# Kernel optimization log

Measured on AMD Instinct MI355X. Metric: run time of the kernel, lower is better.

The kernel has to match this reference:

```python
import jax, jax.numpy as jnp
import numpy as np

# dims
N_USER = 30000; N_ITEM = 30000; HID = 256; HEADS = 4; DH = HID // HEADS
L = 2; E_BUYS = 200000
IMG_D = 512; TASTE_D = 768; NUTR_D = 20; LR = 64; IMG_RANK = 64
EPS = 1e-5
# node type order: 0=user 1=item 2=taste 3=intention 4=image
# edge type order: taste->item, intention->item, image->item, user->item (buys), item->user (bought_by)


def _bn(x, g, b):
    # nn.BatchNorm1d in training mode (biased variance), deterministic
    mu = jnp.mean(x, axis=0)
    var = jnp.mean((x - mu) ** 2, axis=0)
    return (x - mu) * jax.lax.rsqrt(var + EPS) * g + b


def _segment_softmax(logits, seg, n):
    m = jax.ops.segment_max(logits, seg, num_segments=n)
    m = jnp.where(jnp.isfinite(m), m, 0.0)
    e = jnp.exp(logits - m[seg])
    s = jax.ops.segment_sum(e, seg, num_segments=n)
    return e / (s[seg] + 1e-16)


def _model(p, user_id, item_id, buys_src, buys_dst):
    # --- encoders (dropout = identity in eval) ---
    xu = jax.nn.relu(_bn(p['user_emb'][user_id] @ p['user_W'] + p['user_b'], p['user_bn_g'], p['user_bn_b']))
    xi = jax.nn.relu(_bn(p['item_emb'][item_id] @ p['item_W'] + p['item_b'], p['item_bn_g'], p['item_bn_b']))
    ximg = (p['image_feat'] @ p['img_U']) @ p['img_V'] + p['img_b']  # LowRankLinear
    xt = p['taste_feat'] @ p['taste_W'] + p['taste_b']
    xn = p['intent_feat'] @ p['intent_W'] + p['intent_b']
    xs = [xu, xi, xt, xn, ximg]
    assoc = jnp.arange(N_ITEM, dtype=jnp.int32)
    # (src_type, dst_type, src_idx, dst_idx)
    edges = [(2, 1, assoc, assoc), (3, 1, assoc, assoc), (4, 1, assoc, assoc),
             (0, 1, buys_src, buys_dst), (1, 0, buys_dst, buys_src)]
    scale = 1.0 / np.sqrt(DH)
    n_of = [N_USER, N_ITEM]
    for l in range(L):
        k, q, v = [], [], []
        for t in range(5):
            kqv = xs[t] @ p['kqv_W'][l, t] + p['kqv_b'][l, t]
            kk, qq, vv = jnp.split(kqv, 3, axis=1)
            k.append(kk.reshape(-1, HEADS, DH))
            q.append(qq.reshape(-1, HEADS, DH))
            v.append(vv.reshape(-1, HEADS, DH))
        buf = {0: [], 1: []}
        for e, (s, d, si, di) in enumerate(edges):
            # relation-specific per-head transforms of source k/v (all src nodes, then gather)
            ke = jnp.einsum('nhd,hde->nhe', k[s], p['k_rel'][l, e])
            ve = jnp.einsum('nhd,hde->nhe', v[s], p['v_rel'][l, e])
            logit = jnp.sum(q[d][di] * ke[si], axis=-1) * p['p_rel'][l, e] * scale  # [E,H]
            buf[d].append((logit, ve[si], di))
        new_xs = list(xs)
        for d in (0, 1):  # dst node types: user, item
            logits = jnp.concatenate([b[0] for b in buf[d]], axis=0)
            msgs = jnp.concatenate([b[1] for b in buf[d]], axis=0)
            dsts = jnp.concatenate([b[2] for b in buf[d]], axis=0)
            alpha = _segment_softmax(logits, dsts, n_of[d])  # softmax over ALL incoming edges per dst node
            agg = jax.ops.segment_sum(alpha[:, :, None] * msgs, dsts, num_segments=n_of[d])
            o = jax.nn.gelu(agg.reshape(-1, HID), approximate=False) @ p['out_W'][l, d] + p['out_b'][l, d]
            sg = jax.nn.sigmoid(p['skip'][l, d])
            o = sg * o + (1.0 - sg) * xs[d]  # HGTConv learned skip
            o = o + xs[d]                    # MultiModalFusionGAT residual
            o = jax.nn.relu(_bn(o, p['fbn_g'][l, d], p['fbn_b'][l, d]))  # per-type BN+ReLU (dropout eval)
            new_xs[d] = o
        xs = new_xs  # taste/intention/image pass through unchanged
    return jnp.stack(xs, axis=0)  # [5, 30000, HID]


def setup_inputs():
    key = jax.random.key(0)
    ks = iter(jax.random.split(key, 48))
    def nrm(shape, scale=0.05):
        return jax.random.normal(next(ks), shape, dtype=jnp.float32) * scale
    z = lambda *s: jnp.zeros(s, jnp.float32)
    o = lambda *s: jnp.ones(s, jnp.float32)
    inp = {}
    inp['user_id'] = jnp.arange(N_USER, dtype=jnp.int32)
    inp['item_id'] = jnp.arange(N_ITEM, dtype=jnp.int32)
    inp['buys_src'] = jax.random.randint(next(ks), (E_BUYS,), 0, N_USER, dtype=jnp.int32)
    inp['buys_dst'] = jax.random.randint(next(ks), (E_BUYS,), 0, N_ITEM, dtype=jnp.int32)
    inp['image_feat'] = nrm((N_ITEM, IMG_D), 1.0)
    inp['taste_feat'] = nrm((N_ITEM, TASTE_D), 1.0)
    inp['intent_feat'] = nrm((N_ITEM, NUTR_D), 1.0)
    inp['user_emb'] = nrm((N_USER, LR), 0.1)
    inp['user_W'] = nrm((LR, HID)); inp['user_b'] = z(HID)
    inp['user_bn_g'] = o(HID); inp['user_bn_b'] = z(HID)
    inp['item_emb'] = nrm((N_ITEM, LR), 0.1)
    inp['item_W'] = nrm((LR, HID)); inp['item_b'] = z(HID)
    inp['item_bn_g'] = o(HID); inp['item_bn_b'] = z(HID)
    inp['img_U'] = nrm((IMG_D, IMG_RANK)); inp['img_V'] = nrm((IMG_RANK, HID)); inp['img_b'] = z(HID)
    inp['taste_W'] = nrm((TASTE_D, HID)); inp['taste_b'] = z(HID)
    inp['intent_W'] = nrm((NUTR_D, HID)); inp['intent_b'] = z(HID)
    inp['kqv_W'] = nrm((L, 5, HID, 3 * HID)); inp['kqv_b'] = z(L, 5, 3 * HID)
    inp['out_W'] = nrm((L, 5, HID, HID)); inp['out_b'] = z(L, 5, HID)
    inp['k_rel'] = nrm((L, 5, HEADS, DH, DH))
    inp['v_rel'] = nrm((L, 5, HEADS, DH, DH))
    inp['p_rel'] = o(L, 5, HEADS)
    inp['skip'] = o(L, 5)
    inp['fbn_g'] = o(L, 2, HID); inp['fbn_b'] = z(L, 2, HID)
    return inp


def reference(user_id, item_id, buys_src, buys_dst, image_feat, taste_feat, intent_feat,
              user_emb, user_W, user_b, user_bn_g, user_bn_b,
              item_emb, item_W, item_b, item_bn_g, item_bn_b,
              img_U, img_V, img_b, taste_W, taste_b, intent_W, intent_b,
              kqv_W, kqv_b, out_W, out_b, k_rel, v_rel, p_rel, skip, fbn_g, fbn_b):
    p = dict(image_feat=image_feat, taste_feat=taste_feat, intent_feat=intent_feat,
             user_emb=user_emb, user_W=user_W, user_b=user_b, user_bn_g=user_bn_g, user_bn_b=user_bn_b,
             item_emb=item_emb, item_W=item_W, item_b=item_b, item_bn_g=item_bn_g, item_bn_b=item_bn_b,
             img_U=img_U, img_V=img_V, img_b=img_b, taste_W=taste_W, taste_b=taste_b,
             intent_W=intent_W, intent_b=intent_b, kqv_W=kqv_W, kqv_b=kqv_b, out_W=out_W, out_b=out_b,
             k_rel=k_rel, v_rel=v_rel, p_rel=p_rel, skip=skip, fbn_g=fbn_g, fbn_b=fbn_b)
    return _model(p, user_id, item_id, buys_src, buys_dst)
```

## Files before the change

### kernel.cpp

```cpp
#include <hip/hip_runtime.h>
#include <math.h>

#define HID 256
#define EBUY 200000
#define NNODE 30000
#define MP 30080
static const size_t S  = (size_t)NNODE * HID;
static const size_t SP = (size_t)MP * HID;

typedef __attribute__((ext_vector_type(8))) short  short8;
typedef __attribute__((ext_vector_type(4))) float  f32x4;

#define OFF_TASTE 0
#define OFF_INT   196608
#define OFF_IMGU  204800
#define OFF_IMGV  237568
#define OFF_USER  253952
#define OFF_ITEM  270336
#define OFF_OUTW  286720
#define WENC_TOT  548864

__device__ __forceinline__ float gelu_f(float x) {
    return 0.5f * x * (1.0f + erff(x * 0.70710678118654752f));
}
__device__ __forceinline__ unsigned short f2bf(float f) {
    unsigned u = __float_as_uint(f);
    u = (u + 0x7FFFu + ((u >> 16) & 1u)) >> 16;
    return (unsigned short)u;
}
__device__ __forceinline__ float b2f(unsigned short us) {
    return __uint_as_float((unsigned)us << 16);
}

__global__ void conv_pad(const float* __restrict__ in, unsigned short* __restrict__ o,
                         int M, int K, int Kpad)
{
    int i = blockIdx.x * 256 + threadIdx.x;
    if (i >= M * Kpad) return;
    int r = i / Kpad, k = i % Kpad;
    o[i] = (k < K) ? f2bf(in[(size_t)r * K + k]) : (unsigned short)0;
}

__global__ void wtconv_all(const float* __restrict__ taste_W, const float* __restrict__ intent_W,
                           const float* __restrict__ img_U, const float* __restrict__ img_V,
                           const float* __restrict__ user_W, const float* __restrict__ item_W,
                           const float* __restrict__ out_W, unsigned short* __restrict__ WENC)
{
    int i = blockIdx.x * 256 + threadIdx.x;
    if (i >= WENC_TOT) return;
    const float* W; int K, N, Kpad, idx;
    if (i < OFF_INT)        { W = taste_W;  K = 768; N = 256; Kpad = 768; idx = i - OFF_TASTE; }
    else if (i < OFF_IMGU)  { W = intent_W; K = 20;  N = 256; Kpad = 32;  idx = i - OFF_INT; }
    else if (i < OFF_IMGV)  { W = img_U;    K = 512; N = 64;  Kpad = 512; idx = i - OFF_IMGU; }
    else if (i < OFF_USER)  { W = img_V;    K = 64;  N = 256; Kpad = 64;  idx = i - OFF_IMGV; }
    else if (i < OFF_ITEM)  { W = user_W;   K = 64;  N = 256; Kpad = 64;  idx = i - OFF_USER; }
    else if (i < OFF_OUTW)  { W = item_W;   K = 64;  N = 256; Kpad = 64;  idx = i - OFF_ITEM; }
    else {
        int k = (i - OFF_OUTW) >> 16;
        int l = k >> 1, d = k & 1;
        W = out_W + (size_t)(l * 5 + d) * 65536;
        K = 256; N = 256; Kpad = 256; idx = (i - OFF_OUTW) & 65535;
    }
    int n = idx / Kpad, kk = idx % Kpad;
    WENC[i] = (kk < K) ? f2bf(W[(size_t)kk * N + n]) : (unsigned short)0;
}

__global__ void build_kqv(const float* __restrict__ kqv_W, const float* __restrict__ kqv_b,
                          const float* __restrict__ k_rel, const float* __restrict__ v_rel,
                          unsigned short* __restrict__ WKV, float* __restrict__ bKV,
                          unsigned short* __restrict__ WQ, float* __restrict__ bQ)
{
    int s = blockIdx.y;
    int l = s / 5, t = s % 5;
    static const int es[5] = {3, 4, 0, 1, 2};
    int e = es[t];
    int tid = blockIdx.x * 256 + threadIdx.x;
    if (tid >= 257 * 768) return;
    int r = tid / 768, c = tid % 768;
    int cb = c >> 8, cc = c & 255;
    int h = cc >> 6, dd = cc & 63;
    const float* W = kqv_W + (size_t)s * 196608;
    const float* bv = kqv_b + (size_t)s * 768;
    const float* Wrow = (r < 256) ? (W + (size_t)r * 768) : bv;
    if (cb == 1) {
        if (t >= 2) return;
        float outv = Wrow[256 + cc];
        if (r < 256) WQ[(size_t)(l * 2 + t) * 65536 + (size_t)cc * 256 + r] = f2bf(outv);
        else         bQ[(l * 2 + t) * 256 + cc] = outv;
        return;
    }
    const float* R = ((cb == 0) ? k_rel : v_rel) + (size_t)(l * 5 + e) * 16384 + (size_t)h * 4096;
    int sb = (cb == 0) ? 0 : 512;
    float sum = 0.f;
    #pragma unroll 8
    for (int d = 0; d < 64; ++d)
        sum += Wrow[sb + h * 64 + d] * R[d * 64 + dd];
    int col = (cb == 0) ? cc : 256 + cc;
    if (r < 256) WKV[(size_t)s * 131072 + (size_t)col * 256 + r] = f2bf(sum);
    else         bKV[s * 512 + col] = sum;
}

#define KPAD 40
#define OPAD 136
template<int AF32, int GATH2, int BSEL, int EPI>
__launch_bounds__(256)
__global__ void gemm_mfma(const void* __restrict__ Ap, const void* __restrict__ Ap2,
                          const int* __restrict__ g1, const int* __restrict__ g2,
                          const unsigned short* __restrict__ BT0, int bStride,
                          const float* __restrict__ bias0, const float* __restrict__ bias1,
                          int biasStride,
                          float* __restrict__ D0, unsigned short* __restrict__ Db,
                          unsigned short* __restrict__ Db2,
                          int M, int N, int K,
                          const float* __restrict__ skipP, const float* __restrict__ resid,
                          float* __restrict__ bns)
{
    __shared__ union {
        struct { unsigned short A[128 * KPAD]; unsigned short B[128 * KPAD]; } s;
        unsigned short O[128 * OPAD];
    } sm;
    const int tid = threadIdx.x;
    const int gx = gridDim.x;
    int bid = blockIdx.y * gx + blockIdx.x;
    {
        int nwg = gx * gridDim.y;
        int q = nwg >> 3, r = nwg & 7;
        int xc = bid & 7, i = bid >> 3;
        int base = (xc < r) ? xc * (q + 1) : r * (q + 1) + (xc - r) * q;
        bid = base + i;
    }
    const int bx = bid % gx, by = bid / gx;
    const int row0 = by * 128, col0 = bx * 128;
    const int wid = tid >> 6, lane = tid & 63;
    const int wr = wid >> 1, wc = wid & 1;
    const int l16 = lane & 15, kg = lane >> 4;
    const int tt = (BSEL || GATH2) ? (by / 235) : 0;

    const unsigned short* BT = BT0 + (size_t)tt * bStride;
    const float* bias = bias0;
    if (GATH2)              bias = tt ? bias1 : bias0;
    else if (BSEL && bias0) bias = bias0 + (size_t)tt * biasStride;

    f32x4 acc[4][4];
    const f32x4 zero = {0.f, 0.f, 0.f, 0.f};
    #pragma unroll
    for (int i = 0; i < 4; ++i)
        #pragma unroll
        for (int j = 0; j < 4; ++j) acc[i][j] = zero;

    const int rA0 = tid >> 2, rA1 = (tid + 256) >> 2;
    const int q0 = tid & 3;

    const float* Af0 = nullptr; const float* Af1 = nullptr;
    const unsigned short* Ab0 = nullptr; const unsigned short* Ab1 = nullptr;
    if (GATH2) {
        int lr0 = row0 + rA0 - tt * MP; if (lr0 >= NNODE) lr0 = NNODE - 1;
        int lr1 = row0 + rA1 - tt * MP; if (lr1 >= NNODE) lr1 = NNODE - 1;
        const int* gA = tt ? g2 : g1;
        const float* Abase = tt ? (const float*)Ap2 : (const float*)Ap;
        Af0 = Abase + (size_t)gA[lr0] * K;
        Af1 = Abase + (size_t)gA[lr1] * K;
    } else if (AF32) {
        Af0 = (const float*)Ap + (size_t)min(row0 + rA0, M - 1) * K;
        Af1 = (const float*)Ap + (size_t)min(row0 + rA1, M - 1) * K;
    } else {
        Ab0 = (const unsigned short*)Ap + (size_t)min(row0 + rA0, M - 1) * K;
        Ab1 = (const unsigned short*)Ap + (size_t)min(row0 + rA1, M - 1) * K;
    }
    const unsigned short* Bb0 = BT + (size_t)min(col0 + rA0, N - 1) * K;
    const unsigned short* Bb1 = BT + (size_t)min(col0 + rA1, N - 1) * K;

    for (int k0 = 0; k0 < K; k0 += 32) {
        if (AF32 || GATH2) {
            float4 x0 = *(const float4*)&Af0[k0 + q0 * 8];
            float4 x1 = *(const float4*)&Af0[k0 + q0 * 8 + 4];
            float4 y0 = *(const float4*)&Af1[k0 + q0 * 8];
            float4 y1 = *(const float4*)&Af1[k0 + q0 * 8 + 4];
            ushort4 u0 = {f2bf(x0.x), f2bf(x0.y), f2bf(x0.z), f2bf(x0.w)};
            ushort4 u1 = {f2bf(x1.x), f2bf(x1.y), f2bf(x1.z), f2bf(x1.w)};
            ushort4 w0 = {f2bf(y0.x), f2bf(y0.y), f2bf(y0.z), f2bf(y0.w)};
            ushort4 w1 = {f2bf(y1.x), f2bf(y1.y), f2bf(y1.z), f2bf(y1.w)};
            *(ushort4*)&sm.s.A[rA0 * KPAD + q0 * 8]     = u0;
            *(ushort4*)&sm.s.A[rA0 * KPAD + q0 * 8 + 4] = u1;
            *(ushort4*)&sm.s.A[rA1 * KPAD + q0 * 8]     = w0;
            *(ushort4*)&sm.s.A[rA1 * KPAD + q0 * 8 + 4] = w1;
        } else {
            *(uint4*)&sm.s.A[rA0 * KPAD + q0 * 8] = *(const uint4*)&Ab0[k0 + q0 * 8];
            *(uint4*)&sm.s.A[rA1 * KPAD + q0 * 8] = *(const uint4*)&Ab1[k0 + q0 * 8];
        }
        *(uint4*)&sm.s.B[rA0 * KPAD + q0 * 8] = *(const uint4*)&Bb0[k0 + q0 * 8];
        *(uint4*)&sm.s.B[rA1 * KPAD + q0 * 8] = *(const uint4*)&Bb1[k0 + q0 * 8];
        __syncthreads();
        short8 af[4], bfr[4];
        #pragma unroll
        for (int i = 0; i < 4; ++i) {
            af[i]  = *(const short8*)&sm.s.A[(wr * 64 + i * 16 + l16) * KPAD + kg * 8];
            bfr[i] = *(const short8*)&sm.s.B[(wc * 64 + i * 16 + l16) * KPAD + kg * 8];
        }
        #pragma unroll
        for (int i = 0; i < 4; ++i)
            #pragma unroll
            for (int j = 0; j < 4; ++j)
                acc[i][j] = __builtin_amdgcn_mfma_f32_16x16x32_bf16(af[i], bfr[j], acc[i][j], 0, 0, 0);
        __syncthreads();
    }

    float sg = 0.f;
    if (EPI == 2) sg = 1.f / (1.f + __expf(-skipP[0]));
    #pragma unroll
    for (int j = 0; j < 4; ++j) {
        int lc = wc * 64 + j * 16 + l16;
        int cc = col0 + lc;
        float cs = 0.f, cs2 = 0.f;
        float bv = (bias && cc < N) ? bias[cc] : 0.f;
        #pragma unroll
        for (int i = 0; i < 4; ++i) {
            #pragma unroll
            for (int r = 0; r < 4; ++r) {
                int lr = wr * 64 + i * 16 + kg * 4 + r;
                int rr = row0 + lr;
                float v = acc[i][j][r] + bv;
                if (EPI == 0) {
                    if (D0 && cc < N && rr < M) D0[(size_t)rr * N + cc] = v;
                    sm.O[lr * OPAD + lc] = f2bf(v);
                } else if (EPI == 4 || EPI == 5) {
                    sm.O[lr * OPAD + lc] = f2bf(v);
                } else if (EPI == 6) {
                    D0[(size_t)rr * 256 + cc] = v;
                } else if (EPI == 2) {
                    if (rr < M) {
                        float xo = resid[(size_t)rr * 256 + cc];
                        float o = sg * v + (2.f - sg) * xo;
                        D0[(size_t)rr * 256 + cc] = o;
                        cs += o; cs2 += o * o;
                    }
                }
            }
        }
        if (EPI == 2) {
            cs  += __shfl_xor(cs, 16);  cs  += __shfl_xor(cs, 32);
            cs2 += __shfl_xor(cs2, 16); cs2 += __shfl_xor(cs2, 32);
            if (kg == 0 && cc < N) {
                atomicAdd(&bns[cc], cs);
                atomicAdd(&bns[256 + cc], cs2);
            }
        }
    }
    if (EPI == 0 || EPI == 4 || EPI == 5) {
        __syncthreads();
        unsigned short* T; int ldN, cofs;
        if (EPI == 4)      { T = (col0 < 256) ? Db : Db2; ldN = 256; cofs = col0 & 255; }
        else if (EPI == 5) { T = Db; ldN = 256; cofs = col0; }
        else               { T = Db; ldN = N;   cofs = col0; }
        int nloc = N - col0; if (nloc > 128) nloc = 128;
        if (nloc >= 128) {
            int lr = tid >> 1, half = tid & 1;
            int rr = row0 + lr;
            if (EPI != 0 || rr < M) {
                uint4* dst = (uint4*)&T[(size_t)rr * ldN + cofs + half * 64];
                const uint4* srcp = (const uint4*)&sm.O[lr * OPAD + half * 64];
                #pragma unroll
                for (int c = 0; c < 8; ++c) dst[c] = srcp[c];
            }
        } else {
            if (tid < 128) {
                int lr = tid, rr = row0 + lr;
                if (rr < M) {
                    uint4* dst = (uint4*)&T[(size_t)rr * ldN + cofs];
                    const uint4* srcp = (const uint4*)&sm.O[lr * OPAD];
                    #pragma unroll
                    for (int c = 0; c < 8; ++c) dst[c] = srcp[c];
                }
            }
        }
    }
}

__global__ void edge_hist2(const int* __restrict__ dstk, const int* __restrict__ srck,
                           int* __restrict__ cnt)
{
    int j = blockIdx.x * 256 + threadIdx.x;
    if (j < EBUY) atomicAdd(&cnt[dstk[j]], 1);
    else if (j < 2 * EBUY) atomicAdd(&cnt[NNODE + srck[j - EBUY]], 1);
}

#define SCAN_NB 30
#define SCAN_CH 1000
__global__ void scan_part(const int* __restrict__ cnt, int* __restrict__ bt)
{
    int set = blockIdx.y;
    const int* c = cnt + set * NNODE;
    int b = blockIdx.x;
    int i = b * SCAN_CH + threadIdx.x;
    int v = (threadIdx.x < SCAN_CH && i < NNODE) ? c[i] : 0;
    __shared__ int wsum[16];
    int lane = threadIdx.x & 63, wv = threadIdx.x >> 6;
    for (int o = 32; o; o >>= 1) v += __shfl_down(v, o);
    if (lane == 0) wsum[wv] = v;
    __syncthreads();
    if (threadIdx.x == 0) {
        int s = 0;
        for (int w = 0; w < 16; ++w) s += wsum[w];
        bt[set * 32 + b] = s;
    }
}

__global__ void scan_mid(int* __restrict__ bt, int* __restrict__ off_i, int* __restrict__ off_u)
{
    int set = threadIdx.x;
    if (set >= 2) return;
    int* b = bt + set * 32;
    int s = 0;
    for (int i = 0; i < SCAN_NB; ++i) { int c = b[i]; b[i] = s; s += c; }
    (set ? off_u : off_i)[NNODE] = s;
}

__global__ void scan_final(const int* __restrict__ cnt, const int* __restrict__ bt,
                           int* __restrict__ off_i, int* __restrict__ off_u,
                           int* __restrict__ cur_i, int* __restrict__ cur_u)
{
    int set = blockIdx.y;
    const int* c = cnt + set * NNODE;
    int* off = set ? off_u : off_i;
    int* cur = set ? cur_u : cur_i;
    int b = blockIdx.x;
    int i = b * SCAN_CH + threadIdx.x;
    int v = (threadIdx.x < SCAN_CH && i < NNODE) ? c[i] : 0;
    int lane = threadIdx.x & 63, wv = threadIdx.x >> 6;
    int x = v;
    for (int o = 1; o < 64; o <<= 1) { int t = __shfl_up(x, o); if (lane >= o) x += t; }
    __shared__ int wtot[16];
    if (lane == 63) wtot[wv] = x;
    __syncthreads();
    if (wv == 0) {
        int y = (lane < 16) ? wtot[lane] : 0;
        for (int o = 1; o < 16; o <<= 1) { int t = __shfl_up(y, o); if (lane >= o) y += t; }
        if (lane < 16) wtot[lane] = y;
    }
    __syncthreads();
    int wbase = (wv == 0) ? 0 : wtot[wv - 1];
    int excl = bt[set * 32 + b] + wbase + x - v;
    if (threadIdx.x < SCAN_CH && i < NNODE) { off[i] = excl; cur[i] = excl; }
}

__global__ void edge_place2(const int* __restrict__ dstk, const int* __restrict__ srck,
                            int* __restrict__ cur_i, int* __restrict__ cur_u,
                            int* __restrict__ src_i, int* __restrict__ src_u)
{
    int j = blockIdx.x * 256 + threadIdx.x;
    if (j < EBUY) {
        int pos = atomicAdd(&cur_i[dstk[j]], 1);
        src_i[pos] = srck[j];
    } else if (j < 2 * EBUY) {
        int j2 = j - EBUY;
        int pos = atomicAdd(&cur_u[srck[j2]], 1);
        src_u[pos] = dstk[j2];
    }
}

template<int HAS_ASSOC>
__launch_bounds__(256)
__global__ void attn_gather(const unsigned short* __restrict__ Qd,
                            const unsigned short* __restrict__ KEs,
                            const unsigned short* __restrict__ VEs,
                            const unsigned short* __restrict__ KEa,
                            const unsigned short* __restrict__ VEa,
                            const int* __restrict__ roff, const int* __restrict__ srcArr,
                            const float* __restrict__ pR,
                            unsigned short* __restrict__ AGGb)
{
    int wid = (blockIdx.x * 256 + threadIdx.x) >> 6;
    int lane = threadIdx.x & 63;
    if (wid >= NNODE) return;
    int h = lane >> 4;

    ushort4 qb = *(const ushort4*)(Qd + (size_t)wid * 256 + lane * 4);
    float4 q = {b2f(qb.x), b2f(qb.y), b2f(qb.z), b2f(qb.w)};
    float m = -INFINITY, s = 0.f;
    float4 acc = {0.f, 0.f, 0.f, 0.f};

    if (HAS_ASSOC) {
        #pragma unroll
        for (int e = 0; e < 3; ++e) {
            ushort4 kb = *(const ushort4*)(KEa + (size_t)e * SP + (size_t)wid * 256 + lane * 4);
            float d = q.x * b2f(kb.x) + q.y * b2f(kb.y) + q.z * b2f(kb.z) + q.w * b2f(kb.w);
            for (int off = 8; off; off >>= 1) d += __shfl_xor(d, off, 16);
            float lg = d * pR[e * 4 + h] * 0.125f;
            ushort4 vv = *(const ushort4*)(VEa + (size_t)e * SP + (size_t)wid * 256 + lane * 4);
            float mn = fmaxf(m, lg);
            float so = __expf(m - mn);
            float ev = __expf(lg - mn);
            s = s * so + ev;
            acc.x = acc.x * so + ev * b2f(vv.x);
            acc.y = acc.y * so + ev * b2f(vv.y);
            acc.z = acc.z * so + ev * b2f(vv.z);
            acc.w = acc.w * so + ev * b2f(vv.w);
            m = mn;
        }
    }

    float pb = pR[(HAS_ASSOC ? 12 : 16) + h] * 0.125f;
    int j1 = roff[wid + 1];
    for (int j = roff[wid]; j < j1; ++j) {
        int src = srcArr[j];
        ushort4 kb = *(const ushort4*)(KEs + (size_t)src * 256 + lane * 4);
        float d = q.x * b2f(kb.x) + q.y * b2f(kb.y) + q.z * b2f(kb.z) + q.w * b2f(kb.w);
        for (int off = 8; off; off >>= 1) d += __shfl_xor(d, off, 16);
        float lg = d * pb;
        ushort4 vv = *(const ushort4*)(VEs + (size_t)src * 256 + lane * 4);
        float mn = fmaxf(m, lg);
        float so = __expf(m - mn);
        float ev = __expf(lg - mn);
        s = s * so + ev;
        acc.x = acc.x * so + ev * b2f(vv.x);
        acc.y = acc.y * so + ev * b2f(vv.y);
        acc.z = acc.z * so + ev * b2f(vv.z);
        acc.w = acc.w * so + ev * b2f(vv.w);
        m = mn;
    }

    float inv = 1.f / (s + 1e-16f);
    ushort4 o4;
    o4.x = f2bf(gelu_f(acc.x * inv));
    o4.y = f2bf(gelu_f(acc.y * inv));
    o4.z = f2bf(gelu_f(acc.z * inv));
    o4.w = f2bf(gelu_f(acc.w * inv));
    *(ushort4*)(AGGb + (size_t)wid * 256 + lane * 4) = o4;
}

#define BNB 512
__global__ void bn_stats2(const float* __restrict__ SCRf, float* __restrict__ part)
{
    int tt = blockIdx.y;
    const float* x = SCRf + (size_t)tt * SP;
    int col = threadIdx.x;
    int b = blockIdx.x;
    float s = 0.f, s2 = 0.f;
    int r = b;
    for (; r + 3 * BNB < NNODE; r += 4 * BNB) {
        float v0 = x[(size_t)r * 256 + col];
        float v1 = x[(size_t)(r + BNB) * 256 + col];
        float v2 = x[(size_t)(r + 2 * BNB) * 256 + col];
        float v3 = x[(size_t)(r + 3 * BNB) * 256 + col];
        s += v0 + v1 + v2 + v3;
        s2 += v0 * v0 + v1 * v1 + v2 * v2 + v3 * v3;
    }
    for (; r < NNODE; r += BNB) {
        float v = x[(size_t)r * 256 + col];
        s += v; s2 += v * v;
    }
    part[((size_t)tt * BNB + b) * 512 + col] = s;
    part[((size_t)tt * BNB + b) * 512 + 256 + col] = s2;
}

__global__ void bn_fin2(const float* __restrict__ part,
                        const float* __restrict__ g0, const float* __restrict__ b0,
                        const float* __restrict__ g1, const float* __restrict__ b1,
                        float* __restrict__ scsh)
{
    int tid = threadIdx.x;
    int tt = tid >> 8, col = tid & 255;
    const float* p = part + (size_t)tt * BNB * 512;
    float s = 0.f, s2 = 0.f;
    #pragma unroll 4
    for (int b = 0; b < BNB; ++b) { s += p[b * 512 + col]; s2 += p[b * 512 + 256 + col]; }
    float mu = s / (float)NNODE;
    float var = s2 / (float)NNODE - mu * mu;
    float sc = rsqrtf(var + 1e-5f) * (tt ? g1 : g0)[col];
    scsh[tt * 512 + col] = sc;
    scsh[tt * 512 + 256 + col] = (tt ? b1 : b0)[col] - mu * sc;
}

__global__ void bn_apply2(const float* __restrict__ SCRf, const float* __restrict__ scsh,
                          float* __restrict__ out, unsigned short* __restrict__ XBall)
{
    const int Q4 = NNODE * 64;
    for (int i = blockIdx.x * 256 + threadIdx.x; i < 2 * Q4; i += gridDim.x * 256) {
        int tt = (i >= Q4) ? 1 : 0;
        int local = i - tt * Q4;
        int c4 = local & 63;
        float4 sc4 = *(const float4*)&scsh[tt * 512 + c4 * 4];
        float4 sh4 = *(const float4*)&scsh[tt * 512 + 256 + c4 * 4];
        float4 v = ((const float4*)(SCRf + (size_t)tt * SP))[local];
        v.x = fmaxf(v.x * sc4.x + sh4.x, 0.f);
        v.y = fmaxf(v.y * sc4.y + sh4.y, 0.f);
        v.z = fmaxf(v.z * sc4.z + sh4.z, 0.f);
        v.w = fmaxf(v.w * sc4.w + sh4.w, 0.f);
        ((float4*)(out + (size_t)tt * S))[local] = v;
        ushort4 u = {f2bf(v.x), f2bf(v.y), f2bf(v.z), f2bf(v.w)};
        ((ushort4*)(XBall + (size_t)tt * SP))[local] = u;
    }
}

__global__ void bn_find(const float* __restrict__ bns, const float* __restrict__ g,
                        const float* __restrict__ b_, float* __restrict__ scsh)
{
    int col = threadIdx.x;
    float s = bns[col], s2 = bns[256 + col];
    float mu = s / (float)NNODE;
    float var = s2 / (float)NNODE - mu * mu;
    float sc = rsqrtf(var + 1e-5f) * g[col];
    scsh[col] = sc;
    scsh[256 + col] = b_[col] - mu * sc;
}

__global__ void bn_apply1(const float* __restrict__ x, const float* __restrict__ scsh,
                          float* __restrict__ y, unsigned short* __restrict__ yb)
{
    const int Q4 = NNODE * 64;
    int c4 = threadIdx.x & 63;
    float4 sc4 = *(const float4*)&scsh[c4 * 4];
    float4 sh4 = *(const float4*)&scsh[256 + c4 * 4];
    for (int i = blockIdx.x * 256 + threadIdx.x; i < Q4; i += gridDim.x * 256) {
        float4 v = ((const float4*)x)[i];
        v.x = fmaxf(v.x * sc4.x + sh4.x, 0.f);
        v.y = fmaxf(v.y * sc4.y + sh4.y, 0.f);
        v.z = fmaxf(v.z * sc4.z + sh4.z, 0.f);
        v.w = fmaxf(v.w * sc4.w + sh4.w, 0.f);
        ((float4*)y)[i] = v;
        ushort4 u = {f2bf(v.x), f2bf(v.y), f2bf(v.z), f2bf(v.w)};
        ((ushort4*)yb)[i] = u;
    }
}

extern "C" void kernel_launch(void* const* d_in, const int* in_sizes, int n_in,
                              void* d_out, int out_size, void* d_ws, size_t ws_size,
                              hipStream_t stream)
{
    const int*   user_id    = (const int*)d_in[0];
    const int*   item_id    = (const int*)d_in[1];
    const int*   buys_src   = (const int*)d_in[2];
    const int*   buys_dst   = (const int*)d_in[3];
    const float* image_feat = (const float*)d_in[4];
    const float* taste_feat = (const float*)d_in[5];
    const float* intent_feat= (const float*)d_in[6];
    const float* user_emb   = (const float*)d_in[7];
    const float* user_W     = (const float*)d_in[8];
    const float* user_b     = (const float*)d_in[9];
    const float* user_bn_g  = (const float*)d_in[10];
    const float* user_bn_b  = (const float*)d_in[11];
    const float* item_emb   = (const float*)d_in[12];
    const float* item_W     = (const float*)d_in[13];
    const float* item_b     = (const float*)d_in[14];
    const float* item_bn_g  = (const float*)d_in[15];
    const float* item_bn_b  = (const float*)d_in[16];
    const float* img_U      = (const float*)d_in[17];
    const float* img_V      = (const float*)d_in[18];
    const float* img_b      = (const float*)d_in[19];
    const float* taste_W    = (const float*)d_in[20];
    const float* taste_b    = (const float*)d_in[21];
    const float* intent_W   = (const float*)d_in[22];
    const float* intent_b   = (const float*)d_in[23];
    const float* kqv_W      = (const float*)d_in[24];
    const float* kqv_b      = (const float*)d_in[25];
    const float* out_W      = (const float*)d_in[26];
    const float* out_b      = (const float*)d_in[27];
    const float* k_rel      = (const float*)d_in[28];
    const float* v_rel      = (const float*)d_in[29];
    const float* p_rel      = (const float*)d_in[30];
    const float* skip       = (const float*)d_in[31];
    const float* fbn_g      = (const float*)d_in[32];
    const float* fbn_b      = (const float*)d_in[33];

    float* out = (float*)d_out;
    float* ws  = (float*)d_ws;

    float* SCRf = ws;
    float* BNSp = SCRf + 2 * SP;
    float* BNS  = BNSp + 2 * BNB * 512;
    float* SCSH = BNS + 512;
    float* bKV  = SCSH + 1024;
    float* bQ   = bKV + 5120;
    unsigned short* QB    = (unsigned short*)(bQ + 1024);
    unsigned short* XBall = QB + 2 * SP;
    unsigned short* KEall = XBall + 5 * SP;
    unsigned short* VEall = KEall + 5 * SP;
    unsigned short* AGB   = VEall + 5 * SP;
    unsigned short* IMB   = AGB + S;
    unsigned short* IPB   = IMB + (size_t)NNODE * 64;
    unsigned short* WKV   = IPB + (size_t)NNODE * 32;
    unsigned short* WQ    = WKV + 1310720;
    unsigned short* WENC  = WQ + 262144;
    int* cnt   = (int*)(WENC + WENC_TOT);
    int* off_i = cnt + 2 * NNODE;
    int* off_u = off_i + NNODE + 1;
    int* cur_i = off_u + NNODE + 1;
    int* cur_u = cur_i + NNODE;
    int* src_i = cur_u + NNODE;
    int* src_u = src_i + EBUY;
    int* bt    = src_u + EBUY;

    size_t need = (size_t)((char*)(bt + 64) - (char*)ws);
    if (ws_size < need) return;

    hipMemsetAsync(cnt, 0, 2 * NNODE * 4, stream);
    edge_hist2<<<(2 * EBUY + 255) / 256, 256, 0, stream>>>(buys_dst, buys_src, cnt);
    scan_part<<<dim3(SCAN_NB, 2), 1024, 0, stream>>>(cnt, bt);
    scan_mid<<<1, 64, 0, stream>>>(bt, off_i, off_u);
    scan_final<<<dim3(SCAN_NB, 2), 1024, 0, stream>>>(cnt, bt, off_i, off_u, cur_i, cur_u);
    edge_place2<<<(2 * EBUY + 255) / 256, 256, 0, stream>>>(buys_dst, buys_src, cur_i, cur_u, src_i, src_u);

    wtconv_all<<<(WENC_TOT + 255) / 256, 256, 0, stream>>>(taste_W, intent_W, img_U, img_V,
                                                           user_W, item_W, out_W, WENC);
    build_kqv<<<dim3(771, 10), 256, 0, stream>>>(kqv_W, kqv_b, k_rel, v_rel, WKV, bKV, WQ, bQ);
    conv_pad<<<(NNODE * 32 + 255) / 256, 256, 0, stream>>>(intent_feat, IPB, NNODE, 20, 32);

    hipLaunchKernelGGL((gemm_mfma<1,0,0,0>), dim3(2,235), dim3(256), 0, stream,
        taste_feat, nullptr, nullptr, nullptr, WENC + OFF_TASTE, 0, taste_b, nullptr, 0,
        out + 2*S, XBall + 2*SP, nullptr, NNODE, 256, 768, nullptr, nullptr, nullptr);
    hipLaunchKernelGGL((gemm_mfma<0,0,0,0>), dim3(2,235), dim3(256), 0, stream,
        IPB, nullptr, nullptr, nullptr, WENC + OFF_INT, 0, intent_b, nullptr, 0,
        out + 3*S, XBall + 3*SP, nullptr, NNODE, 256, 32, nullptr, nullptr, nullptr);
    hipLaunchKernelGGL((gemm_mfma<1,0,0,0>), dim3(1,235), dim3(256), 0, stream,
        image_feat, nullptr, nullptr, nullptr, WENC + OFF_IMGU, 0, nullptr, nullptr, 0,
        nullptr, IMB, nullptr, NNODE, 64, 512, nullptr, nullptr, nullptr);
    hipLaunchKernelGGL((gemm_mfma<0,0,0,0>), dim3(2,235), dim3(256), 0, stream,
        IMB, nullptr, nullptr, nullptr, WENC + OFF_IMGV, 0, img_b, nullptr, 0,
        out + 4*S, XBall + 4*SP, nullptr, NNODE, 256, 64, nullptr, nullptr, nullptr);
    hipLaunchKernelGGL((gemm_mfma<1,1,1,6>), dim3(2,470), dim3(256), 0, stream,
        user_emb, item_emb, user_id, item_id, WENC + OFF_USER, 16384, user_b, item_b, 0,
        SCRf, nullptr, nullptr, 2*MP, 256, 64, nullptr, nullptr, nullptr);
    bn_stats2<<<dim3(BNB, 2), 256, 0, stream>>>(SCRf, BNSp);
    bn_fin2<<<1, 512, 0, stream>>>(BNSp, user_bn_g, user_bn_b, item_bn_g, item_bn_b, SCSH);
    bn_apply2<<<960, 256, 0, stream>>>(SCRf, SCSH, out, XBall);

    for (int l = 0; l < 2; ++l) {
        hipLaunchKernelGGL((gemm_mfma<0,0,1,4>), dim3(4, 5*235), dim3(256), 0, stream,
            XBall, nullptr, nullptr, nullptr, WKV + (size_t)l*5*131072, 131072,
            bKV + l*5*512, nullptr, 512, nullptr, KEall, VEall,
            5*MP, 512, 256, nullptr, nullptr, nullptr);
        hipLaunchKernelGGL((gemm_mfma<0,0,1,5>), dim3(2, 2*235), dim3(256), 0, stream,
            XBall, nullptr, nullptr, nullptr, WQ + (size_t)l*2*65536, 65536,
            bQ + l*2*256, nullptr, 256, nullptr, QB, nullptr,
            2*MP, 256, 256, nullptr, nullptr, nullptr);
        hipLaunchKernelGGL((attn_gather<1>), dim3((NNODE*64 + 255)/256), dim3(256), 0, stream,
            QB + SP, KEall, VEall, KEall + 2*SP, VEall + 2*SP, off_i, src_i,
            p_rel + l*20, AGB);
        hipMemsetAsync(BNS, 0, 512 * 4, stream);
        hipLaunchKernelGGL((gemm_mfma<0,0,0,2>), dim3(2,235), dim3(256), 0, stream,
            AGB, nullptr, nullptr, nullptr, WENC + OFF_OUTW + (size_t)(l*2+1)*65536, 0,
            out_b + (l*5+1)*256, nullptr, 0, SCRf, nullptr, nullptr,
            NNODE, 256, 256, skip + (l*5+1), out + S, BNS);
        bn_find<<<1, 256, 0, stream>>>(BNS, fbn_g + (l*2+1)*256, fbn_b + (l*2+1)*256, SCSH);
        bn_apply1<<<960, 256, 0, stream>>>(SCRf, SCSH, out + S, XBall + SP);
        hipLaunchKernelGGL((attn_gather<0>), dim3((NNODE*64 + 255)/256), dim3(256), 0, stream,
            QB, KEall + SP, VEall + SP, nullptr, nullptr, off_u, src_u,
            p_rel + l*20, AGB);
        hipMemsetAsync(BNS, 0, 512 * 4, stream);
        hipLaunchKernelGGL((gemm_mfma<0,0,0,2>), dim3(2,235), dim3(256), 0, stream,
            AGB, nullptr, nullptr, nullptr, WENC + OFF_OUTW + (size_t)(l*2+0)*65536, 0,
            out_b + (l*5+0)*256, nullptr, 0, SCRf, nullptr, nullptr,
            NNODE, 256, 256, skip + (l*5+0), out, BNS);
        bn_find<<<1, 256, 0, stream>>>(BNS, fbn_g + (l*2+0)*256, fbn_b + (l*2+0)*256, SCSH);
        bn_apply1<<<960, 256, 0, stream>>>(SCRf, SCSH, out, XBall);
    }
}
```

Before: 1.085 ms.

## Double-buffer GEMM LDS tiles with direct global-to-LDS loads and swizzled epilogue

Reworks the MFMA GEMM main loop to double-buffer A and B tiles in shared memory. The bf16 operands now use global_load_lds so the next K-slice loads while the current one feeds the MFMAs, and one of the two barriers per iteration is removed. The padded LDS layout is replaced by an unpadded 32-wide layout, and the output staging buffer uses an XOR swizzle instead of padding. The unpadded operand layout may bring LDS bank conflicts on the fragment reads. The f32 A path is still synchronous, and the single barrier per iteration relies on global_load_lds completion ordering.

```diff
diff --git a/kernel.cpp b/kernel.cpp
--- a/kernel.cpp
+++ b/kernel.cpp
@@ -30,6 +30,11 @@
 }
 __device__ __forceinline__ float b2f(unsigned short us) {
     return __uint_as_float((unsigned)us << 16);
+}
+__device__ __forceinline__ void gl_lds16(const unsigned short* g, unsigned short* l) {
+    __builtin_amdgcn_global_load_lds(
+        (const __attribute__((address_space(1))) unsigned int*)g,
+        (__attribute__((address_space(3))) unsigned int*)l, 16, 0, 0);
 }
 
 __global__ void conv_pad(const float* __restrict__ in, unsigned short* __restrict__ o,
@@ -100,8 +105,6 @@
     else         bKV[s * 512 + col] = sum;
 }
 
-#define KPAD 40
-#define OPAD 136
 template<int AF32, int GATH2, int BSEL, int EPI>
 __launch_bounds__(256)
 __global__ void gemm_mfma(const void* __restrict__ Ap, const void* __restrict__ Ap2,
@@ -116,8 +119,8 @@
                           float* __restrict__ bns)
 {
     __shared__ union {
-        struct { unsigned short A[128 * KPAD]; unsigned short B[128 * KPAD]; } s;
-        unsigned short O[128 * OPAD];
+        unsigned short AB[4][4096];
+        unsigned short O[16384];
     } sm;
     const int tid = threadIdx.x;
     const int gx = gridDim.x;
@@ -148,11 +151,18 @@
         #pragma unroll
         for (int j = 0; j < 4; ++j) acc[i][j] = zero;
 
-    const int rA0 = tid >> 2, rA1 = (tid + 256) >> 2;
+    const int lrow = lane >> 2, lchk = lane & 3;
+    int cB0 = min(col0 + wid * 32 + lrow, N - 1);
+    int cB1 = min(col0 + wid * 32 + 16 + lrow, N - 1);
+    const unsigned short* Bp0 = BT + (size_t)cB0 * K + lchk * 8;
+    const unsigned short* Bp1 = BT + (size_t)cB1 * K + lchk * 8;
+    const int ofs0 = wid * 1024;
+    const int ofs1 = wid * 1024 + 512;
+
+    const unsigned short* Ap0b = nullptr; const unsigned short* Ap1b = nullptr;
+    const float* Af0 = nullptr; const float* Af1 = nullptr;
+    const int rA0 = tid >> 2, rA1 = (tid >> 2) + 64;
     const int q0 = tid & 3;
-
-    const float* Af0 = nullptr; const float* Af1 = nullptr;
-    const unsigned short* Ab0 = nullptr; const unsigned short* Ab1 = nullptr;
     if (GATH2) {
         int lr0 = row0 + rA0 - tt * MP; if (lr0 >= NNODE) lr0 = NNODE - 1;
         int lr1 = row0 + rA1 - tt * MP; if (lr1 >= NNODE) lr1 = NNODE - 1;
@@ -164,38 +174,45 @@
         Af0 = (const float*)Ap + (size_t)min(row0 + rA0, M - 1) * K;
         Af1 = (const float*)Ap + (size_t)min(row0 + rA1, M - 1) * K;
     } else {
-        Ab0 = (const unsigned short*)Ap + (size_t)min(row0 + rA0, M - 1) * K;
-        Ab1 = (const unsigned short*)Ap + (size_t)min(row0 + rA1, M - 1) * K;
-    }
-    const unsigned short* Bb0 = BT + (size_t)min(col0 + rA0, N - 1) * K;
-    const unsigned short* Bb1 = BT + (size_t)min(col0 + rA1, N - 1) * K;
-
-    for (int k0 = 0; k0 < K; k0 += 32) {
-        if (AF32 || GATH2) {
-            float4 x0 = *(const float4*)&Af0[k0 + q0 * 8];
-            float4 x1 = *(const float4*)&Af0[k0 + q0 * 8 + 4];
-            float4 y0 = *(const float4*)&Af1[k0 + q0 * 8];
-            float4 y1 = *(const float4*)&Af1[k0 + q0 * 8 + 4];
-            ushort4 u0 = {f2bf(x0.x), f2bf(x0.y), f2bf(x0.z), f2bf(x0.w)};
-            ushort4 u1 = {f2bf(x1.x), f2bf(x1.y), f2bf(x1.z), f2bf(x1.w)};
-            ushort4 w0 = {f2bf(y0.x), f2bf(y0.y), f2bf(y0.z), f2bf(y0.w)};
-            ushort4 w1 = {f2bf(y1.x), f2bf(y1.y), f2bf(y1.z), f2bf(y1.w)};
-            *(ushort4*)&sm.s.A[rA0 * KPAD + q0 * 8]     = u0;
-            *(ushort4*)&sm.s.A[rA0 * KPAD + q0 * 8 + 4] = u1;
-            *(ushort4*)&sm.s.A[rA1 * KPAD + q0 * 8]     = w0;
-            *(ushort4*)&sm.s.A[rA1 * KPAD + q0 * 8 + 4] = w1;
-        } else {
-            *(uint4*)&sm.s.A[rA0 * KPAD + q0 * 8] = *(const uint4*)&Ab0[k0 + q0 * 8];
-            *(uint4*)&sm.s.A[rA1 * KPAD + q0 * 8] = *(const uint4*)&Ab1[k0 + q0 * 8];
-        }
-        *(uint4*)&sm.s.B[rA0 * KPAD + q0 * 8] = *(const uint4*)&Bb0[k0 + q0 * 8];
-        *(uint4*)&sm.s.B[rA1 * KPAD + q0 * 8] = *(const uint4*)&Bb1[k0 + q0 * 8];
-        __syncthreads();
+        int rr0 = min(row0 + wid * 32 + lrow, M - 1);
+        int rr1 = min(row0 + wid * 32 + 16 + lrow, M - 1);
+        Ap0b = (const unsigned short*)Ap + (size_t)rr0 * K + lchk * 8;
+        Ap1b = (const unsigned short*)Ap + (size_t)rr1 * K + lchk * 8;
+    }
+
+    const int nt = K >> 5;
+    int cur = 0;
+    #define STAGE(c, k0) do { \
+        if (AF32 || GATH2) { \
+            float4 x0 = *(const float4*)&Af0[(k0) + q0 * 8]; \
+            float4 x1 = *(const float4*)&Af0[(k0) + q0 * 8 + 4]; \
+            float4 y0 = *(const float4*)&Af1[(k0) + q0 * 8]; \
+            float4 y1 = *(const float4*)&Af1[(k0) + q0 * 8 + 4]; \
+            ushort4 u0 = {f2bf(x0.x), f2bf(x0.y), f2bf(x0.z), f2bf(x0.w)}; \
+            ushort4 u1 = {f2bf(x1.x), f2bf(x1.y), f2bf(x1.z), f2bf(x1.w)}; \
+            ushort4 w0 = {f2bf(y0.x), f2bf(y0.y), f2bf(y0.z), f2bf(y0.w)}; \
+            ushort4 w1 = {f2bf(y1.x), f2bf(y1.y), f2bf(y1.z), f2bf(y1.w)}; \
+            *(ushort4*)&sm.AB[c][rA0 * 32 + q0 * 8]     = u0; \
+            *(ushort4*)&sm.AB[c][rA0 * 32 + q0 * 8 + 4] = u1; \
+            *(ushort4*)&sm.AB[c][rA1 * 32 + q0 * 8]     = w0; \
+            *(ushort4*)&sm.AB[c][rA1 * 32 + q0 * 8 + 4] = w1; \
+        } else { \
+            gl_lds16(Ap0b + (k0), &sm.AB[c][ofs0]); \
+            gl_lds16(Ap1b + (k0), &sm.AB[c][ofs1]); \
+        } \
+        gl_lds16(Bp0 + (k0), &sm.AB[2 + (c)][ofs0]); \
+        gl_lds16(Bp1 + (k0), &sm.AB[2 + (c)][ofs1]); \
+    } while (0)
+
+    STAGE(0, 0);
+    __syncthreads();
+    for (int s = 0; s < nt; ++s) {
+        if (s + 1 < nt) STAGE(cur ^ 1, (s + 1) * 32);
         short8 af[4], bfr[4];
         #pragma unroll
         for (int i = 0; i < 4; ++i) {
-            af[i]  = *(const short8*)&sm.s.A[(wr * 64 + i * 16 + l16) * KPAD + kg * 8];
-            bfr[i] = *(const short8*)&sm.s.B[(wc * 64 + i * 16 + l16) * KPAD + kg * 8];
+            af[i]  = *(const short8*)&sm.AB[cur][(wr * 64 + i * 16 + l16) * 32 + kg * 8];
+            bfr[i] = *(const short8*)&sm.AB[2 + cur][(wc * 64 + i * 16 + l16) * 32 + kg * 8];
         }
         #pragma unroll
         for (int i = 0; i < 4; ++i)
@@ -203,7 +220,9 @@
             for (int j = 0; j < 4; ++j)
                 acc[i][j] = __builtin_amdgcn_mfma_f32_16x16x32_bf16(af[i], bfr[j], acc[i][j], 0, 0, 0);
         __syncthreads();
-    }
+        cur ^= 1;
+    }
+    #undef STAGE
 
     float sg = 0.f;
     if (EPI == 2) sg = 1.f / (1.f + __expf(-skipP[0]));
@@ -222,9 +241,9 @@
                 float v = acc[i][j][r] + bv;
                 if (EPI == 0) {
                     if (D0 && cc < N && rr < M) D0[(size_t)rr * N + cc] = v;
-                    sm.O[lr * OPAD + lc] = f2bf(v);
+                    sm.O[lr * 128 + ((((lc >> 3) ^ (lr & 7)) << 3) | (lc & 7))] = f2bf(v);
                 } else if (EPI == 4 || EPI == 5) {
-                    sm.O[lr * OPAD + lc] = f2bf(v);
+                    sm.O[lr * 128 + ((((lc >> 3) ^ (lr & 7)) << 3) | (lc & 7))] = f2bf(v);
                 } else if (EPI == 6) {
                     D0[(size_t)rr * 256 + cc] = v;
                 } else if (EPI == 2) {
@@ -258,18 +277,20 @@
             int rr = row0 + lr;
             if (EPI != 0 || rr < M) {
                 uint4* dst = (uint4*)&T[(size_t)rr * ldN + cofs + half * 64];
-                const uint4* srcp = (const uint4*)&sm.O[lr * OPAD + half * 64];
                 #pragma unroll
-                for (int c = 0; c < 8; ++c) dst[c] = srcp[c];
+                for (int c = 0; c < 8; ++c) {
+                    int ch = half * 8 + c;
+                    dst[c] = *(const uint4*)&sm.O[lr * 128 + ((ch ^ (lr & 7)) << 3)];
+                }
             }
         } else {
             if (tid < 128) {
                 int lr = tid, rr = row0 + lr;
                 if (rr < M) {
                     uint4* dst = (uint4*)&T[(size_t)rr * ldN + cofs];
-                    const uint4* srcp = (const uint4*)&sm.O[lr * OPAD];
                     #pragma unroll
-                    for (int c = 0; c < 8; ++c) dst[c] = srcp[c];
+                    for (int c = 0; c < 8; ++c)
+                        dst[c] = *(const uint4*)&sm.O[lr * 128 + ((c ^ (lr & 7)) << 3)];
                 }
             }
         }
```

Measured after the change: 1.085 ms. Within noise of the previous version (+0.0%).
